# Kernel optimization log

Measured on AMD Instinct MI355X. Metric: run time of the kernel, lower is better.

Reference implementation:

```python
import jax, jax.numpy as jnp
import numpy as np

HEAD_DIM = 128
ROPE_THETA = 10000.0


def _rope_cos_sin(positions, head_dim, theta):
    # positions: [T] int -> cos/sin [T, head_dim] (LLaMA half-split convention)
    inv_freq = 1.0 / (theta ** (jnp.arange(0, head_dim, 2, dtype=jnp.float32) / head_dim))
    ang = positions.astype(jnp.float32)[:, None] * inv_freq  # [T, D/2]
    cos = jnp.concatenate([jnp.cos(ang), jnp.cos(ang)], axis=-1)
    sin = jnp.concatenate([jnp.sin(ang), jnp.sin(ang)], axis=-1)
    return cos, sin


def _apply_rope(x, cos, sin):
    # x: [T, H, D]; rotate_half: (-x2, x1)
    half = x.shape[-1] // 2
    rot = jnp.concatenate([-x[..., half:], x[..., :half]], axis=-1)
    return x * cos[:, None, :] + rot * sin[:, None, :]


def setup_inputs() -> dict:
    key = jax.random.key(0)
    ks = jax.random.split(key, 5)
    T, hid = 4096, 4096
    S = 1024  # equal-length sequences -> B = T // S = 4
    Hq, Hk, D = 32, 8, HEAD_DIM
    hidden = jax.random.normal(ks[0], (T, hid), dtype=jnp.float32)
    positions = (jnp.arange(T, dtype=jnp.int32) % S)
    q_w = jax.random.normal(ks[1], (Hq * D, hid), dtype=jnp.float32) * 0.02
    k_w = jax.random.normal(ks[2], (Hk * D, hid), dtype=jnp.float32) * 0.02
    v_w = jax.random.normal(ks[3], (Hk * D, hid), dtype=jnp.float32) * 0.02
    o_w = jax.random.normal(ks[4], (hid, Hq * D), dtype=jnp.float32) * 0.02
    return {"hidden": hidden, "positions": positions, "q_w": q_w, "k_w": k_w,
            "v_w": v_w, "o_w": o_w, "seq_len": S}


def reference(hidden, positions, q_w, k_w, v_w, o_w, seq_len):
    T, hid = hidden.shape
    D = HEAD_DIM
    Hq = q_w.shape[0] // D
    Hk = k_w.shape[0] // D
    G = Hq // Hk  # num_kv_groups
    S = int(seq_len)
    B = T // S
    # QKV projections (ColumnParallel, tp=1): y = x @ W^T
    q = (hidden @ q_w.T).reshape(T, Hq, D)
    k = (hidden @ k_w.T).reshape(T, Hk, D)
    v = (hidden @ v_w.T).reshape(T, Hk, D)
    # fused RoPE on q and k
    cos, sin = _rope_cos_sin(positions, D, ROPE_THETA)
    q = _apply_rope(q, cos, sin)
    k = _apply_rope(k, cos, sin)
    # varlen (equal-length) causal GQA attention
    q = q.reshape(B, S, Hk, G, D)
    k = k.reshape(B, S, Hk, D)
    v = v.reshape(B, S, Hk, D)
    scale = 1.0 / np.sqrt(D).astype(np.float32)
    scores = jnp.einsum('bqhgd,bkhd->bhgqk', q, k) * scale  # [B,Hk,G,S,S]
    causal = jnp.tril(jnp.ones((S, S), dtype=bool))
    scores = jnp.where(causal, scores, jnp.asarray(-1e30, scores.dtype))
    attn = jax.nn.softmax(scores, axis=-1)
    out = jnp.einsum('bhgqk,bkhd->bqhgd', attn, v).reshape(T, Hq * D)
    # output projection (RowParallel, tp=1)
    return out @ o_w.T
```

## Files before the change

### kernel.cpp

```cpp
#include <hip/hip_runtime.h>
#include <hip/hip_bf16.h>

typedef __attribute__((ext_vector_type(8))) short bf16x8;
typedef __attribute__((ext_vector_type(4))) float f32x4;
typedef __attribute__((ext_vector_type(8))) unsigned short u16x8;

__device__ inline unsigned short f2bf(float f) {
  unsigned u = __builtin_bit_cast(unsigned, f);
  u += 0x7FFFu + ((u >> 16) & 1u);
  return (unsigned short)(u >> 16);
}
__device__ inline float b2f(unsigned short h) {
  unsigned u = ((unsigned)h) << 16;
  return __builtin_bit_cast(float, u);
}

typedef const __attribute__((address_space(1))) void* gas_ptr;
typedef __attribute__((address_space(3))) void* las_ptr;
__device__ inline void load_lds16(const void* g, void* l) {
  __builtin_amdgcn_global_load_lds((gas_ptr)g, (las_ptr)l, 16, 0, 0);
}

#define PHB() do { asm volatile("" ::: "memory"); __builtin_amdgcn_s_barrier(); \
                   __builtin_amdgcn_sched_barrier(0); } while (0)
#define PHB_MID() do { asm volatile("" ::: "memory"); __builtin_amdgcn_s_barrier(); } while (0)

__global__ __launch_bounds__(256) void cvt_f32_bf16(const float* __restrict__ src,
                                                    unsigned short* __restrict__ dst,
                                                    int n4) {
  int i = blockIdx.x * 256 + threadIdx.x;
  if (i >= n4) return;
  float4 v = ((const float4*)src)[i];
  ushort4 o;
  o.x = f2bf(v.x); o.y = f2bf(v.y); o.z = f2bf(v.z); o.w = f2bf(v.w);
  ((ushort4*)dst)[i] = o;
}

template <int NLOADS>
__device__ inline void stage_tile(const unsigned short* __restrict__ g, int ld,
                                  size_t grow0, int kcol0, char* ldsdst, int tid) {
#pragma unroll
  for (int i = 0; i < NLOADS; ++i) {
    int c = tid + i * 512;
    int r = c >> 3;
    int k = (c & 7) ^ (r & 7);
    load_lds16(g + (grow0 + r) * ld + kcol0 + k * 8, ldsdst + c * 16);
  }
}

__device__ inline void xcd_decode(int orig, int nTM, int nTN, int& bm, int& bn) {
  int x = orig & 7, i = orig >> 3;
  int xr = x >> 1, xc = x & 1;
  int bmch = nTM >> 2, bnch = nTN >> 1;
  bm = xr * bmch + i / bnch;
  bn = xc * bnch + i % bnch;
}

template <int Kc, int Nc, int Mc, bool OUT_F32>
__global__ __launch_bounds__(512, 1) void gemmT(const unsigned short* __restrict__ A,
                                                const unsigned short* __restrict__ B,
                                                void* __restrict__ Cv) {
  __shared__ __attribute__((aligned(16))) char lds[147456];
  const int tid = threadIdx.x;
  const int wave = tid >> 6, lane = tid & 63;
  const int l15 = lane & 15, l4 = lane >> 4;
  const int wr = wave >> 2, wc = wave & 3;
  int bm, bn;
  xcd_decode(blockIdx.x, Mc >> 7, Nc >> 8, bm, bn);
  const size_t rowA0 = (size_t)bm << 7, rowB0 = (size_t)bn << 8;
  const int nt = Kc >> 6;

  stage_tile<2>(A, Kc, rowA0, 0,  lds + 0,             tid);
  stage_tile<4>(B, Kc, rowB0, 0,  lds + 16384,         tid);
  stage_tile<2>(A, Kc, rowA0, 64, lds + 49152,         tid);
  stage_tile<4>(B, Kc, rowB0, 64, lds + 49152 + 16384, tid);
  asm volatile("s_waitcnt vmcnt(6)" ::: "memory");
  __builtin_amdgcn_s_barrier();
  __builtin_amdgcn_sched_barrier(0);

  f32x4 acc[4][4] = {};

#pragma unroll 3
  for (int t = 0; t < nt; ++t) {
    char* cbuf = lds + (t % 3) * 49152;
    char* sbuf = lds + ((t + 2) % 3) * 49152;
    const char* bufA = cbuf;
    const char* bufB = cbuf + 16384;
    const int kc2 = (t + 2) << 6;

    bf16x8 af[4][2], bf[4][2];

#pragma unroll
    for (int m = 0; m < 4; ++m) {
      int row = wr * 64 + m * 16 + l15;
#pragma unroll
      for (int kk = 0; kk < 2; ++kk)
        af[m][kk] = *(const bf16x8*)(bufA + (row << 7) + (((kk * 4 + l4) ^ (row & 7)) << 4));
    }
#pragma unroll
    for (int n = 0; n < 2; ++n) {
      int row = wc * 64 + n * 16 + l15;
#pragma unroll
      for (int kk = 0; kk < 2; ++kk)
        bf[n][kk] = *(const bf16x8*)(bufB + (row << 7) + (((kk * 4 + l4) ^ (row & 7)) << 4));
    }
    if (t < nt - 2) stage_tile<4>(B, Kc, rowB0, kc2, sbuf + 16384, tid);
    __builtin_amdgcn_s_barrier();
    asm volatile("s_waitcnt lgkmcnt(0)" ::: "memory");
    __builtin_amdgcn_sched_barrier(0);
    __builtin_amdgcn_s_setprio(1);
#pragma unroll
    for (int m = 0; m < 4; ++m)
#pragma unroll
      for (int n = 0; n < 2; ++n)
#pragma unroll
        for (int kk = 0; kk < 2; ++kk)
          acc[m][n] = __builtin_amdgcn_mfma_f32_16x16x32_bf16(af[m][kk], bf[n][kk], acc[m][n], 0, 0, 0);
    __builtin_amdgcn_s_setprio(0);
    PHB();

#pragma unroll
    for (int n = 2; n < 4; ++n) {
      int row = wc * 64 + n * 16 + l15;
#pragma unroll
      for (int kk = 0; kk < 2; ++kk)
        bf[n][kk] = *(const bf16x8*)(bufB + (row << 7) + (((kk * 4 + l4) ^ (row & 7)) << 4));
    }
    if (t < nt - 2) stage_tile<2>(A, Kc, rowA0, kc2, sbuf, tid);
    if (t <= nt - 3) { asm volatile("s_waitcnt vmcnt(6)" ::: "memory"); }
    else             { asm volatile("s_waitcnt vmcnt(0)" ::: "memory"); }
    __builtin_amdgcn_s_barrier();
    asm volatile("s_waitcnt lgkmcnt(0)" ::: "memory");
    __builtin_amdgcn_sched_barrier(0);
    __builtin_amdgcn_s_setprio(1);
#pragma unroll
    for (int m = 0; m < 4; ++m)
#pragma unroll
      for (int n = 2; n < 4; ++n)
#pragma unroll
        for (int kk = 0; kk < 2; ++kk)
          acc[m][n] = __builtin_amdgcn_mfma_f32_16x16x32_bf16(af[m][kk], bf[n][kk], acc[m][n], 0, 0, 0);
    __builtin_amdgcn_s_setprio(0);
    PHB();
  }

#pragma unroll
  for (int m = 0; m < 4; ++m)
#pragma unroll
    for (int n = 0; n < 4; ++n)
#pragma unroll
      for (int r = 0; r < 4; ++r) {
        size_t row = rowA0 + wr * 64 + m * 16 + l4 * 4 + r;
        size_t col = rowB0 + wc * 64 + n * 16 + l15;
        float v = acc[m][n][r];
        if (OUT_F32) ((float*)Cv)[row * Nc + col] = v;
        else         ((unsigned short*)Cv)[row * Nc + col] = f2bf(v);
      }
}

__device__ inline void stage_half(const unsigned short* __restrict__ g, int ld,
                                  size_t grow0, int kcol0, char* ldsdst, int tid) {
#pragma unroll
  for (int i = 0; i < 2; ++i) {
    int c = tid + i * 512;
    int r = c >> 3;
    int k = (c & 7) ^ (r & 7);
    load_lds16(g + (grow0 + r) * ld + kcol0 + k * 8, ldsdst + c * 16);
  }
}

template <int Kc, int Nc, int Mc, bool OUT_F32>
__global__ __launch_bounds__(512, 2) void gemm8(const unsigned short* __restrict__ A,
                                                const unsigned short* __restrict__ B,
                                                void* __restrict__ Cv) {
  __shared__ __attribute__((aligned(16))) char lds[131072];
  const int tid = threadIdx.x;
  const int wave = tid >> 6, lane = tid & 63;
  const int l15 = lane & 15, l4 = lane >> 4, swz = l15 & 7;
  const int wr = wave >> 2, wc = wave & 3;
  int bm, bn;
  xcd_decode(blockIdx.x, Mc >> 8, Nc >> 8, bm, bn);
  const size_t rowA0 = (size_t)bm << 8, rowB0 = (size_t)bn << 8;
  const int nt = Kc >> 6;
  const int brow = (wc & 1) * 64;

  stage_half(A, Kc, rowA0,       0,  lds + 0,             tid);
  stage_half(A, Kc, rowA0 + 128, 0,  lds + 16384,         tid);
  stage_half(B, Kc, rowB0,       0,  lds + 32768,         tid);
  stage_half(B, Kc, rowB0 + 128, 0,  lds + 49152,         tid);
  stage_half(B, Kc, rowB0,       64, lds + 65536 + 32768, tid);
  stage_half(A, Kc, rowA0,       64, lds + 65536,         tid);
  stage_half(A, Kc, rowA0 + 128, 64, lds + 65536 + 16384, tid);
  asm volatile("s_waitcnt vmcnt(6)" ::: "memory");
  __builtin_amdgcn_s_barrier();
  __builtin_amdgcn_sched_barrier(0);

  f32x4 acc[8][4] = {};
  bf16x8 bf01[2][2];
  {
    const char* bufB0 = lds + 32768 + (wc >> 1) * 16384;
#pragma unroll
    for (int n = 0; n < 2; ++n)
#pragma unroll
      for (int kk = 0; kk < 2; ++kk)
        bf01[n][kk] = *(const bf16x8*)(bufB0 + ((brow + n * 16 + l15) << 7) + (((kk * 4 + l4) ^ swz) << 4));
  }

#pragma unroll 2
  for (int t = 0; t < nt; ++t) {
    char* cbuf = lds + (t & 1) * 65536;
    char* obuf = lds + ((t + 1) & 1) * 65536;
    const char* bufA = cbuf + wr * 16384;
    const char* bufB = cbuf + 32768 + (wc >> 1) * 16384;
    const int kc1 = (t + 1) << 6, kc2 = (t + 2) << 6;

    bf16x8 af[8][2], bf23[2][2];

#pragma unroll
    for (int m = 0; m < 4; ++m)
#pragma unroll
      for (int kk = 0; kk < 2; ++kk)
        af[m][kk] = *(const bf16x8*)(bufA + ((m * 16 + l15) << 7) + (((kk * 4 + l4) ^ swz) << 4));
    if (t < nt - 1) stage_half(B, Kc, rowB0 + 128, kc1, obuf + 49152, tid);
    PHB_MID();
    __builtin_amdgcn_s_setprio(1);
#pragma unroll
    for (int m = 0; m < 4; ++m)
#pragma unroll
      for (int n = 0; n < 2; ++n)
#pragma unroll
        for (int kk = 0; kk < 2; ++kk)
          acc[m][n] = __builtin_amdgcn_mfma_f32_16x16x32_bf16(af[m][kk], bf01[n][kk], acc[m][n], 0, 0, 0);
    __builtin_amdgcn_s_setprio(0);
    PHB();

#pragma unroll
    for (int n = 0; n < 2; ++n)
#pragma unroll
      for (int kk = 0; kk < 2; ++kk)
        bf23[n][kk] = *(const bf16x8*)(bufB + ((brow + (n + 2) * 16 + l15) << 7) + (((kk * 4 + l4) ^ swz) << 4));
    PHB_MID();
    __builtin_amdgcn_s_setprio(1);
#pragma unroll
    for (int m = 0; m < 4; ++m)
#pragma unroll
      for (int n = 0; n < 2; ++n)
#pragma unroll
        for (int kk = 0; kk < 2; ++kk)
          acc[m][n + 2] = __builtin_amdgcn_mfma_f32_16x16x32_bf16(af[m][kk], bf23[n][kk], acc[m][n + 2], 0, 0, 0);
    __builtin_amdgcn_s_setprio(0);
    PHB();

#pragma unroll
    for (int m = 4; m < 8; ++m)
#pragma unroll
      for (int kk = 0; kk < 2; ++kk)
        af[m][kk] = *(const bf16x8*)(bufA + ((m * 16 + l15) << 7) + (((kk * 4 + l4) ^ swz) << 4));
    if (t < nt - 2) stage_half(B, Kc, rowB0, kc2, cbuf + 32768, tid);
    PHB_MID();
    __builtin_amdgcn_s_setprio(1);
#pragma unroll
    for (int m = 4; m < 8; ++m)
#pragma unroll
      for (int n = 0; n < 2; ++n)
#pragma unroll
        for (int kk = 0; kk < 2; ++kk)
          acc[m][n] = __builtin_amdgcn_mfma_f32_16x16x32_bf16(af[m][kk], bf01[n][kk], acc[m][n], 0, 0, 0);
    __builtin_amdgcn_s_setprio(0);
    PHB();

    if (t < nt - 2) {
      stage_half(A, Kc, rowA0,       kc2, cbuf,         tid);
      stage_half(A, Kc, rowA0 + 128, kc2, cbuf + 16384, tid);
    }
    if (t <= nt - 3) { asm volatile("s_waitcnt vmcnt(8)" ::: "memory"); }
    else             { asm volatile("s_waitcnt vmcnt(0)" ::: "memory"); }
    PHB_MID();
    if (t < nt - 1) {
      const char* bufB1 = obuf + 32768 + (wc >> 1) * 16384;
#pragma unroll
      for (int n = 0; n < 2; ++n)
#pragma unroll
        for (int kk = 0; kk < 2; ++kk)
          bf01[n][kk] = *(const bf16x8*)(bufB1 + ((brow + n * 16 + l15) << 7) + (((kk * 4 + l4) ^ swz) << 4));
    }
    __builtin_amdgcn_s_setprio(1);
#pragma unroll
    for (int m = 4; m < 8; ++m)
#pragma unroll
      for (int n = 0; n < 2; ++n)
#pragma unroll
        for (int kk = 0; kk < 2; ++kk)
          acc[m][n + 2] = __builtin_amdgcn_mfma_f32_16x16x32_bf16(af[m][kk], bf23[n][kk], acc[m][n + 2], 0, 0, 0);
    __builtin_amdgcn_s_setprio(0);
    PHB();
  }

#pragma unroll
  for (int m = 0; m < 8; ++m)
#pragma unroll
    for (int n = 0; n < 4; ++n)
#pragma unroll
      for (int r = 0; r < 4; ++r) {
        size_t row = rowA0 + wr * 128 + m * 16 + l4 * 4 + r;
        size_t col = rowB0 + wc * 64 + n * 16 + l15;
        float v = acc[m][n][r];
        if (OUT_F32) ((float*)Cv)[row * Nc + col] = v;
        else         ((unsigned short*)Cv)[row * Nc + col] = f2bf(v);
      }
}

__global__ __launch_bounds__(256) void rope_kernel(unsigned short* __restrict__ qkv,
                                                   const int* __restrict__ positions) {
  int gw = (blockIdx.x * 256 + threadIdx.x) >> 6;
  int lane = threadIdx.x & 63;
  int t = gw / 40, h = gw % 40;
  size_t col0 = (h < 32) ? ((size_t)h << 7) : (4096 + ((size_t)(h - 32) << 7));
  unsigned short* p = qkv + (size_t)t * 6144 + col0;
  float pos = (float)positions[t];
  float inv = powf(10000.0f, -(float)lane * (1.0f / 64.0f));
  float ang = pos * inv;
  float s, c;
  sincosf(ang, &s, &c);
  float x1 = b2f(p[lane]);
  float x2 = b2f(p[lane + 64]);
  p[lane]      = f2bf(x1 * c - x2 * s);
  p[lane + 64] = f2bf(x2 * c + x1 * s);
}

__global__ __launch_bounds__(256, 4) void attn_kernel(const unsigned short* __restrict__ qkv,
                                                      unsigned short* __restrict__ ao) {
  int orig = blockIdx.x;
  int wgid = (orig & 7) * 128 + (orig >> 3);
  int pair = wgid & 7;
  int hq = (wgid >> 3) & 31;
  int b  = wgid >> 8;
  int hk = hq >> 2;
  int tid = threadIdx.x, wave = tid >> 6, lane = tid & 63;
  int l15 = lane & 15, l4 = lane >> 4;

  __shared__ __attribute__((aligned(16))) char ldsA[16384];
  __shared__ __attribute__((aligned(16))) unsigned short Vt[128][72];
  unsigned short (*Ks)[128]    = (unsigned short (*)[128])ldsA;
  unsigned short (*Ps)[16][72] = (unsigned short (*)[16][72])ldsA;

  const float scale = 0.08838834764831845f;

#pragma unroll 1
  for (int iq = 0; iq < 2; ++iq) {
    const int qa = iq ? (15 - pair) : pair;
    const size_t qrow0 = (size_t)(b * 1024 + qa * 64 + wave * 16);

    bf16x8 qf[4];
    {
      const unsigned short* qp = qkv + (qrow0 + l15) * 6144 + ((size_t)hq << 7) + l4 * 8;
#pragma unroll
      for (int kc = 0; kc < 4; ++kc) qf[kc] = *(const bf16x8*)(qp + kc * 32);
    }

    float m_i[4], l_i[4];
    f32x4 oacc[8];
#pragma unroll
    for (int r = 0; r < 4; ++r) { m_i[r] = -1e30f; l_i[r] = 0.0f; }
#pragma unroll
    for (int d = 0; d < 8; ++d) oacc[d] = f32x4{0.f, 0.f, 0.f, 0.f};

#pragma unroll 1
    for (int kt = 0; kt <= qa; ++kt) {
      __syncthreads();

      const unsigned short* kbase = qkv + (size_t)(b * 1024 + kt * 64) * 6144 + 4096 + ((size_t)hk << 7);
#pragma unroll
      for (int j = 0; j < 4; ++j) {
        int c = (j * 4 + wave) * 64 + lane;
        int r = c >> 4;
        int cc = (c & 15) ^ (r & 7);
        load_lds16(kbase + (size_t)r * 6144 + cc * 8, ldsA + c * 16);
      }
      {
        const unsigned short* vp = qkv + (size_t)(b * 1024 + kt * 64 + lane) * 6144 + 5120 + ((size_t)hk << 7) + wave * 32;
        u16x8 va0 = *(const u16x8*)(vp);
        u16x8 va1 = *(const u16x8*)(vp + 8);
        u16x8 va2 = *(const u16x8*)(vp + 16);
        u16x8 va3 = *(const u16x8*)(vp + 24);
        int d0 = wave * 32;
#pragma unroll
        for (int c = 0; c < 8; ++c) Vt[d0 + c][lane]      = va0[c];
#pragma unroll
        for (int c = 0; c < 8; ++c) Vt[d0 + 8 + c][lane]  = va1[c];
#pragma unroll
        for (int c = 0; c < 8; ++c) Vt[d0 + 16 + c][lane] = va2[c];
#pragma unroll
        for (int c = 0; c < 8; ++c) Vt[d0 + 24 + c][lane] = va3[c];
      }
      __syncthreads();

      float pbuf[4][4];
      float tmax[4] = {-1e30f, -1e30f, -1e30f, -1e30f};
#pragma unroll
      for (int nt = 0; nt < 4; ++nt) {
        f32x4 sacc = {0.f, 0.f, 0.f, 0.f};
        int row = nt * 16 + l15;
#pragma unroll
        for (int kc = 0; kc < 4; ++kc) {
          const unsigned short* kp = &Ks[0][0] + row * 128 + (((kc * 4 + l4) ^ (row & 7)) * 8);
          bf16x8 kf = *(const bf16x8*)kp;
          sacc = __builtin_amdgcn_mfma_f32_16x16x32_bf16(qf[kc], kf, sacc, 0, 0, 0);
        }
#pragma unroll
        for (int r = 0; r < 4; ++r) {
          float s = sacc[r] * scale;
          if (kt == qa) {
            int kcol = nt * 16 + l15;
            int qrow = wave * 16 + l4 * 4 + r;
            if (kcol > qrow) s = -1e30f;
          }
          pbuf[nt][r] = s;
          tmax[r] = fmaxf(tmax[r], s);
        }
      }
      __syncthreads();

#pragma unroll
      for (int r = 0; r < 4; ++r) {
        float v = tmax[r];
        v = fmaxf(v, __shfl_xor(v, 1));
        v = fmaxf(v, __shfl_xor(v, 2));
        v = fmaxf(v, __shfl_xor(v, 4));
        v = fmaxf(v, __shfl_xor(v, 8));
        tmax[r] = v;
      }
      float rescale[4];
#pragma unroll
      for (int r = 0; r < 4; ++r) {
        float mn = fmaxf(m_i[r], tmax[r]);
        rescale[r] = __expf(m_i[r] - mn);
        m_i[r] = mn;
      }
      float psum[4] = {0.f, 0.f, 0.f, 0.f};
#pragma unroll
      for (int nt = 0; nt < 4; ++nt)
#pragma unroll
        for (int r = 0; r < 4; ++r) {
          float p = __expf(pbuf[nt][r] - m_i[r]);
          pbuf[nt][r] = p;
          psum[r] += p;
        }
#pragma unroll
      for (int r = 0; r < 4; ++r) {
        float v = psum[r];
        v += __shfl_xor(v, 1);
        v += __shfl_xor(v, 2);
        v += __shfl_xor(v, 4);
        v += __shfl_xor(v, 8);
        l_i[r] = l_i[r] * rescale[r] + v;
      }
#pragma unroll
      for (int d = 0; d < 8; ++d)
#pragma unroll
        for (int r = 0; r < 4; ++r) oacc[d][r] *= rescale[r];

#pragma unroll
      for (int nt = 0; nt < 4; ++nt)
#pragma unroll
        for (int r = 0; r < 4; ++r)
          Ps[wave][l4 * 4 + r][nt * 16 + l15] = f2bf(pbuf[nt][r]);

#pragma unroll
      for (int h = 0; h < 2; ++h) {
        bf16x8 pa = *(const bf16x8*)&Ps[wave][l15][h * 32 + l4 * 8];
#pragma unroll
        for (int d = 0; d < 8; ++d) {
          bf16x8 vf = *(const bf16x8*)&Vt[d * 16 + l15][h * 32 + l4 * 8];
          oacc[d] = __builtin_amdgcn_mfma_f32_16x16x32_bf16(pa, vf, oacc[d], 0, 0, 0);
        }
      }
    }

#pragma unroll
    for (int d = 0; d < 8; ++d)
#pragma unroll
      for (int r = 0; r < 4; ++r) {
        size_t row = qrow0 + l4 * 4 + r;
        size_t col = ((size_t)hq << 7) + d * 16 + l15;
        ao[row * 4096 + col] = f2bf(oacc[d][r] / l_i[r]);
      }
  }
}

extern "C" void kernel_launch(void* const* d_in, const int* in_sizes, int n_in,
                              void* d_out, int out_size, void* d_ws, size_t ws_size,
                              hipStream_t stream) {
  const float* hidden    = (const float*)d_in[0];
  const int*   positions = (const int*)d_in[1];
  const float* q_w       = (const float*)d_in[2];
  const float* k_w       = (const float*)d_in[3];
  const float* v_w       = (const float*)d_in[4];
  const float* o_w       = (const float*)d_in[5];
  float* out = (float*)d_out;

  char* ws = (char*)d_ws;
  unsigned short* hidB  = (unsigned short*)(ws);
  unsigned short* wqkvB = (unsigned short*)(ws + 33554432);
  unsigned short* woB   = (unsigned short*)(ws + 83886080);
  unsigned short* qkvB  = (unsigned short*)(ws + 117440512);
  unsigned short* aoB   = (unsigned short*)(ws + 167772160);

  cvt_f32_bf16<<<16384, 256, 0, stream>>>(hidden, hidB, 4194304);
  cvt_f32_bf16<<<16384, 256, 0, stream>>>(q_w, wqkvB, 4194304);
  cvt_f32_bf16<<<4096, 256, 0, stream>>>(k_w, wqkvB + 16777216, 1048576);
  cvt_f32_bf16<<<4096, 256, 0, stream>>>(v_w, wqkvB + 20971520, 1048576);
  cvt_f32_bf16<<<16384, 256, 0, stream>>>(o_w, woB, 4194304);

  gemmT<4096, 6144, 4096, false><<<768, 512, 0, stream>>>(hidB, wqkvB, (void*)qkvB);

  rope_kernel<<<40960, 256, 0, stream>>>(qkvB, positions);

  attn_kernel<<<1024, 256, 0, stream>>>(qkvB, aoB);

  gemm8<4096, 4096, 4096, true><<<256, 512, 0, stream>>>(aoB, woB, (void*)out);
}
```

Baseline: 521.8 us.

## Simplify QKV GEMM pipeline to one barrier per K-tile with upfront prefetch

Replaces the two-phase ping-pong schedule of the QKV GEMM (split B fragment loads, interleaved staging, priority boosts, and two barriers per K step) with a simpler loop. Each iteration issues both global-to-LDS prefetches up front, loads all A/B fragments, runs all 32 MFMAs, then waits and barriers once. This cuts barrier and scheduling overhead but gives up the fine-grained overlap between LDS reads and MFMA issue, and it relies on the compiler's own scheduling.

New measurement: 524.1 us. About the same (+0.4%).

```diff
diff --git a/kernel.cpp b/kernel.cpp
--- a/kernel.cpp
+++ b/kernel.cpp
@@ -57,7 +57,7 @@
 }
 
 template <int Kc, int Nc, int Mc, bool OUT_F32>
-__global__ __launch_bounds__(512, 1) void gemmT(const unsigned short* __restrict__ A,
+__global__ __launch_bounds__(512, 1) void gemmP(const unsigned short* __restrict__ A,
                                                 const unsigned short* __restrict__ B,
                                                 void* __restrict__ Cv) {
   __shared__ __attribute__((aligned(16))) char lds[147456];
@@ -76,20 +76,22 @@
   stage_tile<4>(B, Kc, rowB0, 64, lds + 49152 + 16384, tid);
   asm volatile("s_waitcnt vmcnt(6)" ::: "memory");
   __builtin_amdgcn_s_barrier();
-  __builtin_amdgcn_sched_barrier(0);
 
   f32x4 acc[4][4] = {};
 
 #pragma unroll 3
   for (int t = 0; t < nt; ++t) {
-    char* cbuf = lds + (t % 3) * 49152;
+    const char* bufA = lds + (t % 3) * 49152;
+    const char* bufB = bufA + 16384;
     char* sbuf = lds + ((t + 2) % 3) * 49152;
-    const char* bufA = cbuf;
-    const char* bufB = cbuf + 16384;
     const int kc2 = (t + 2) << 6;
 
+    if (t < nt - 2) {
+      stage_tile<4>(B, Kc, rowB0, kc2, sbuf + 16384, tid);
+      stage_tile<2>(A, Kc, rowA0, kc2, sbuf, tid);
+    }
+
     bf16x8 af[4][2], bf[4][2];
-
 #pragma unroll
     for (int m = 0; m < 4; ++m) {
       int row = wr * 64 + m * 16 + l15;
@@ -98,50 +100,26 @@
         af[m][kk] = *(const bf16x8*)(bufA + (row << 7) + (((kk * 4 + l4) ^ (row & 7)) << 4));
     }
 #pragma unroll
-    for (int n = 0; n < 2; ++n) {
+    for (int n = 0; n < 4; ++n) {
       int row = wc * 64 + n * 16 + l15;
 #pragma unroll
       for (int kk = 0; kk < 2; ++kk)
         bf[n][kk] = *(const bf16x8*)(bufB + (row << 7) + (((kk * 4 + l4) ^ (row & 7)) << 4));
     }
-    if (t < nt - 2) stage_tile<4>(B, Kc, rowB0, kc2, sbuf + 16384, tid);
-    __builtin_amdgcn_s_barrier();
-    asm volatile("s_waitcnt lgkmcnt(0)" ::: "memory");
-    __builtin_amdgcn_sched_barrier(0);
-    __builtin_amdgcn_s_setprio(1);
+
 #pragma unroll
     for (int m = 0; m < 4; ++m)
 #pragma unroll
-      for (int n = 0; n < 2; ++n)
+      for (int n = 0; n < 4; ++n)
 #pragma unroll
         for (int kk = 0; kk < 2; ++kk)
           acc[m][n] = __builtin_amdgcn_mfma_f32_16x16x32_bf16(af[m][kk], bf[n][kk], acc[m][n], 0, 0, 0);
-    __builtin_amdgcn_s_setprio(0);
-    PHB();
-
-#pragma unroll
-    for (int n = 2; n < 4; ++n) {
-      int row = wc * 64 + n * 16 + l15;
-#pragma unroll
-      for (int kk = 0; kk < 2; ++kk)
-        bf[n][kk] = *(const bf16x8*)(bufB + (row << 7) + (((kk * 4 + l4) ^ (row & 7)) << 4));
-    }
-    if (t < nt - 2) stage_tile<2>(A, Kc, rowA0, kc2, sbuf, tid);
+
     if (t <= nt - 3) { asm volatile("s_waitcnt vmcnt(6)" ::: "memory"); }
     else             { asm volatile("s_waitcnt vmcnt(0)" ::: "memory"); }
+    asm volatile("" ::: "memory");
     __builtin_amdgcn_s_barrier();
-    asm volatile("s_waitcnt lgkmcnt(0)" ::: "memory");
-    __builtin_amdgcn_sched_barrier(0);
-    __builtin_amdgcn_s_setprio(1);
-#pragma unroll
-    for (int m = 0; m < 4; ++m)
-#pragma unroll
-      for (int n = 2; n < 4; ++n)
-#pragma unroll
-        for (int kk = 0; kk < 2; ++kk)
-          acc[m][n] = __builtin_amdgcn_mfma_f32_16x16x32_bf16(af[m][kk], bf[n][kk], acc[m][n], 0, 0, 0);
-    __builtin_amdgcn_s_setprio(0);
-    PHB();
+    asm volatile("" ::: "memory");
   }
 
 #pragma unroll
@@ -512,7 +490,7 @@
   cvt_f32_bf16<<<4096, 256, 0, stream>>>(v_w, wqkvB + 20971520, 1048576);
   cvt_f32_bf16<<<16384, 256, 0, stream>>>(o_w, woB, 4194304);
 
-  gemmT<4096, 6144, 4096, false><<<768, 512, 0, stream>>>(hidB, wqkvB, (void*)qkvB);
+  gemmP<4096, 6144, 4096, false><<<768, 512, 0, stream>>>(hidB, wqkvB, (void*)qkvB);
 
   rope_kernel<<<40960, 256, 0, stream>>>(qkvB, positions);
 
```
